# Optimization experiments

Hardware: AMD Instinct MI355X
Metric: run time of the kernel (lower is better)

Reference implementation:

```python
import jax, jax.numpy as jnp
import numpy as np

B, NUM, FEAT, H = 32, 512, 1024, 8
HLEN = FEAT // H  # 128


def setup_inputs() -> dict:
    key = jax.random.key(0)
    ks = jax.random.split(key, 9)
    x1 = jax.random.normal(ks[0], (B, NUM, FEAT), dtype=jnp.float32)
    x2 = jax.random.normal(ks[1], (B, NUM, FEAT), dtype=jnp.float32)
    adj = jax.random.uniform(ks[2], (B, NUM, NUM), dtype=jnp.float32)
    bias = jax.random.normal(ks[3], (B, NUM, NUM), dtype=jnp.float32)
    mask = jax.random.bernoulli(ks[4], 0.1, (B, 1, NUM, NUM))  # bool
    # per-head projection weights: FCNet([feat, hdim], '', 0.1) == Linear(feat, hdim)
    Wq = jax.random.normal(ks[5], (H, FEAT, HLEN), dtype=jnp.float32) * (1.0 / np.sqrt(FEAT))
    bq = jnp.zeros((H, HLEN), dtype=jnp.float32)
    # output FCNet([feat, feat], 'ReLU', 0.1) == Linear(feat, feat) + ReLU
    Wl = jax.random.normal(ks[6], (FEAT, FEAT), dtype=jnp.float32) * (1.0 / np.sqrt(FEAT))
    bl = jnp.zeros((FEAT,), dtype=jnp.float32)
    return {"x1": x1, "x2": x2, "adj": adj, "bias": bias, "mask": mask,
            "Wq": Wq, "bq": bq, "Wl": Wl, "bl": bl}


def reference(x1, x2, adj, bias, mask, Wq, bq, Wl, bl):
    # adj and bias are unused in the original forward.
    Bsz, num, feat = x1.shape
    h_len = feat // H
    # Q: concat of per-head Linear(feat, h_len) projections -> [B, num, feat],
    # then split into H heads of h_len: [B, H, num, h_len]
    Q = jnp.einsum('bnf,hfd->bhnd', x1, Wq) + bq[None, :, None, :]
    # K = V = x1 reshaped into heads
    K = x1.reshape(Bsz, num, H, h_len).transpose(0, 2, 1, 3)  # [B,H,num,h_len]
    V = K
    # gate: average pool x2 over its sequence dim -> [B, feat] -> [B,H,1,h_len]
    gate = jnp.mean(x2, axis=1).reshape(Bsz, 1, H, h_len).transpose(0, 2, 1, 3)
    scale = 1.0 / np.sqrt(float(h_len))
    aff = jnp.einsum('bhnd,bhmd->bhnm', Q * gate, K * gate) * scale
    L = jnp.where(mask, jnp.float32(-1e9), aff)
    att = jax.nn.softmax(L, axis=3)  # [B,H,num,num]
    V_ = jnp.einsum('bhnm,bhmd->bhnd', att, V)
    V_ = V_.transpose(0, 2, 1, 3).reshape(Bsz, num, feat)
    xout = jax.nn.relu(V_ @ Wl + bl) + x1
    return (xout, att)
```

## Files before the change

### kernel.cpp

```cpp
#include <hip/hip_runtime.h>
#include <hip/hip_bf16.h>

typedef __attribute__((ext_vector_type(8))) short s8v;
typedef __attribute__((ext_vector_type(4))) float f4v;
typedef __hip_bfloat16 bf16;

__device__ __forceinline__ unsigned short f2b(float f) {
  bf16 h = __float2bfloat16(f);
  return *reinterpret_cast<unsigned short*>(&h);
}

__device__ __forceinline__ void gload16(const void* g, void* l) {
  __builtin_amdgcn_global_load_lds(
      (const __attribute__((address_space(1))) void*)g,
      (__attribute__((address_space(3))) void*)l, 16, 0, 0);
}

__global__ __launch_bounds__(256) void gate_kernel(const float* __restrict__ x2,
                                                   float* __restrict__ g2s) {
  __shared__ float red[256];
  const int b = blockIdx.x >> 4, fc = blockIdx.x & 15;
  const int fi = threadIdx.x & 63, ng = threadIdx.x >> 6;
  const int f = fc * 64 + fi;
  const float* p = x2 + (size_t)b * 524288 + f;
  float s = 0.f;
  for (int n = ng * 128; n < ng * 128 + 128; ++n) s += p[(size_t)n * 1024];
  red[threadIdx.x] = s;
  __syncthreads();
  if (threadIdx.x < 64) {
    float tot = red[fi] + red[fi + 64] + red[fi + 128] + red[fi + 192];
    float mean = tot * (1.0f / 512.0f);
    g2s[b * 1024 + f] = mean * mean * 0.08838834764831845f;
  }
}

__global__ __launch_bounds__(256) void cvt_f32_bf16(const float* __restrict__ in,
                                                    bf16* __restrict__ out, int n4) {
  int i = blockIdx.x * 256 + threadIdx.x;
  if (i >= n4) return;
  f4v v = reinterpret_cast<const f4v*>(in)[i];
  ushort4 o;
  o.x = f2b(v.x); o.y = f2b(v.y); o.z = f2b(v.z); o.w = f2b(v.w);
  reinterpret_cast<ushort4*>(out)[i] = o;
}

__global__ __launch_bounds__(256) void transpose_f32_bf16(
    const float* __restrict__ in, bf16* __restrict__ out,
    int in_rstride, int out_rstride, int hi_shift,
    long hi_mul, long lo_mul, long out_mul) {
  __shared__ float tile[32][33];
  const int z = blockIdx.z;
  const long in_off = (long)(z >> hi_shift) * hi_mul + (long)(z & ((1 << hi_shift) - 1)) * lo_mul;
  const int r0 = blockIdx.x * 32, c0 = blockIdx.y * 32;
  const int i = threadIdx.x >> 5, j = threadIdx.x & 31;
  const float* ip = in + in_off + (long)r0 * in_rstride + c0;
#pragma unroll
  for (int s = 0; s < 4; ++s) tile[i + s * 8][j] = ip[(long)(i + s * 8) * in_rstride + j];
  __syncthreads();
  bf16* op = out + (long)z * out_mul + (long)c0 * out_rstride + r0;
#pragma unroll
  for (int s = 0; s < 4; ++s) op[(long)(i + s * 8) * out_rstride + j] = __float2bfloat16(tile[j][i + s * 8]);
}

template <int EPI>
__global__ __launch_bounds__(256) void gemm_nt(
    const bf16* __restrict__ A, const bf16* __restrict__ BT, void* __restrict__ Op,
    const float* __restrict__ e1, const float* __restrict__ e2) {
  __shared__ alignas(16) bf16 As[128 * 32];
  __shared__ alignas(16) bf16 Bs[128 * 32];
  const int t = threadIdx.x;
  const int lane = t & 63;
  const int wv = t >> 6;
  const int wr = wv >> 1, wc = wv & 1;
  const int lr = lane & 15, g = lane >> 4;
  const int o = blockIdx.x;
  const int wk = (o & 7) * 128 + (o >> 3);
  const int m0 = (wk >> 3) * 128, n0 = (wk & 7) * 128;

  const int cr = lane >> 2;
  const int q = (lane & 3) ^ ((lane >> 3) & 3);
  const int c0 = 2 * wv, c1 = 2 * wv + 1;
  const bf16* gA0 = A + (size_t)(m0 + c0 * 16 + cr) * 1024 + q * 8;
  const bf16* gA1 = A + (size_t)(m0 + c1 * 16 + cr) * 1024 + q * 8;
  const bf16* gB0 = BT + (size_t)(n0 + c0 * 16 + cr) * 1024 + q * 8;
  const bf16* gB1 = BT + (size_t)(n0 + c1 * 16 + cr) * 1024 + q * 8;
  bf16* lA0 = &As[c0 * 512]; bf16* lA1 = &As[c1 * 512];
  bf16* lB0 = &Bs[c0 * 512]; bf16* lB1 = &Bs[c1 * 512];

  f4v acc[4][4];
#pragma unroll
  for (int i = 0; i < 4; ++i)
#pragma unroll
    for (int j = 0; j < 4; ++j) acc[i][j] = (f4v){0.f, 0.f, 0.f, 0.f};

  const int xr = (lr >> 1) & 3;

  for (int k0 = 0; k0 < 1024; k0 += 32) {
    __syncthreads();
    gload16(gA0 + k0, lA0);
    gload16(gA1 + k0, lA1);
    gload16(gB0 + k0, lB0);
    gload16(gB1 + k0, lB1);
    __syncthreads();
    s8v af[4], bfr[4];
#pragma unroll
    for (int mi = 0; mi < 4; ++mi)
      af[mi] = *reinterpret_cast<const s8v*>(&As[(wr * 64 + mi * 16 + lr) * 32 + ((g ^ xr) * 8)]);
#pragma unroll
    for (int ni = 0; ni < 4; ++ni)
      bfr[ni] = *reinterpret_cast<const s8v*>(&Bs[(wc * 64 + ni * 16 + lr) * 32 + ((g ^ xr) * 8)]);
#pragma unroll
    for (int mi = 0; mi < 4; ++mi)
#pragma unroll
      for (int ni = 0; ni < 4; ++ni)
        acc[mi][ni] = __builtin_amdgcn_mfma_f32_16x16x32_bf16(af[mi], bfr[ni], acc[mi][ni], 0, 0, 0);
  }

#pragma unroll
  for (int mi = 0; mi < 4; ++mi) {
#pragma unroll
    for (int ni = 0; ni < 4; ++ni) {
#pragma unroll
      for (int v = 0; v < 4; ++v) {
        int row = m0 + wr * 64 + mi * 16 + g * 4 + v;
        int col = n0 + wc * 64 + ni * 16 + lr;
        float val = acc[mi][ni][v];
        if constexpr (EPI == 0) {
          float qv = (val + e1[col]) * e2[(row >> 9) * 1024 + col];
          reinterpret_cast<bf16*>(Op)[(size_t)row * 1024 + col] = __float2bfloat16(qv);
        } else {
          float r2 = fmaxf(val + e1[col], 0.f) + e2[(size_t)row * 1024 + col];
          reinterpret_cast<float*>(Op)[(size_t)row * 1024 + col] = r2;
        }
      }
    }
  }
}

__device__ __forceinline__ int fsw(int r) { return ((r >> 2) | ((r & 1) << 2)); }

__global__ __launch_bounds__(256) void attn_fused(
    const bf16* __restrict__ Qs, const bf16* __restrict__ x1b,
    const bf16* __restrict__ VT, const int* __restrict__ mask,
    float* __restrict__ att, bf16* __restrict__ Vout) {
  __shared__ bf16 P[4][16 * 512];
  const int o = blockIdx.x;
  const int wk = (o & 7) * 256 + (o >> 3);
  const int rt = wk & 7, bh = wk >> 3;
  const int h = bh & 7, b = bh >> 3;
  const int wv = threadIdx.x >> 6;
  const int lane = threadIdx.x & 63;
  const int lr = lane & 15, g = lane >> 4;
  const int n0 = rt * 64 + wv * 16;

  const bf16* qrow = Qs + (size_t)(b * 512 + n0 + lr) * 1024 + h * 128;
  s8v a[4];
#pragma unroll
  for (int kt = 0; kt < 4; ++kt) a[kt] = *reinterpret_cast<const s8v*>(qrow + kt * 32 + g * 8);

  f4v acc[32];
#pragma unroll
  for (int mt = 0; mt < 32; ++mt) acc[mt] = (f4v){0.f, 0.f, 0.f, 0.f};

  const bf16* kbase = x1b + (size_t)b * 524288 + h * 128;
#pragma unroll
  for (int mt = 0; mt < 32; ++mt) {
    const bf16* krow = kbase + (size_t)(mt * 16 + lr) * 1024;
#pragma unroll
    for (int kt = 0; kt < 4; ++kt) {
      s8v bb = *reinterpret_cast<const s8v*>(krow + kt * 32 + g * 8);
      acc[mt] = __builtin_amdgcn_mfma_f32_16x16x32_bf16(a[kt], bb, acc[mt], 0, 0, 0);
    }
  }

  const int* mrow = mask + (size_t)b * 262144 + (size_t)n0 * 512;
  float mx[4] = {-3e38f, -3e38f, -3e38f, -3e38f};
#pragma unroll
  for (int mt = 0; mt < 32; ++mt) {
#pragma unroll
    for (int v = 0; v < 4; ++v) {
      int row = g * 4 + v, col = mt * 16 + lr;
      float val = acc[mt][v];
      val = mrow[row * 512 + col] ? -1e9f : val;
      acc[mt][v] = val;
      mx[v] = fmaxf(mx[v], val);
    }
  }
#pragma unroll
  for (int v = 0; v < 4; ++v) {
    float m = mx[v];
    m = fmaxf(m, __shfl_xor(m, 1));
    m = fmaxf(m, __shfl_xor(m, 2));
    m = fmaxf(m, __shfl_xor(m, 4));
    m = fmaxf(m, __shfl_xor(m, 8));
    mx[v] = m;
  }
  float sm[4] = {0.f, 0.f, 0.f, 0.f};
#pragma unroll
  for (int mt = 0; mt < 32; ++mt) {
#pragma unroll
    for (int v = 0; v < 4; ++v) {
      float e = __expf(acc[mt][v] - mx[v]);
      acc[mt][v] = e;
      sm[v] += e;
    }
  }
#pragma unroll
  for (int v = 0; v < 4; ++v) {
    float s = sm[v];
    s += __shfl_xor(s, 1);
    s += __shfl_xor(s, 2);
    s += __shfl_xor(s, 4);
    s += __shfl_xor(s, 8);
    sm[v] = 1.0f / s;
  }

  float* orow = att + ((size_t)bh * 512 + n0) * 512;
  bf16* Pw = P[wv];
#pragma unroll
  for (int mt = 0; mt < 32; ++mt) {
#pragma unroll
    for (int v = 0; v < 4; ++v) {
      int r = g * 4 + v, c = mt * 16 + lr;
      float tv = acc[mt][v] * sm[v];
      orow[r * 512 + c] = tv;
      Pw[r * 512 + (c ^ (fsw(r) * 8))] = __float2bfloat16(tv);
    }
  }

  s8v a2[16];
  const int fx = fsw(lr) * 8;
#pragma unroll
  for (int kt = 0; kt < 16; ++kt)
    a2[kt] = *reinterpret_cast<const s8v*>(&Pw[lr * 512 + ((kt * 32 + g * 8) ^ fx)]);

  const bf16* vbase = VT + (size_t)bh * 65536;
#pragma unroll
  for (int nt = 0; nt < 8; ++nt) {
    f4v oacc = (f4v){0.f, 0.f, 0.f, 0.f};
#pragma unroll
    for (int kt = 0; kt < 16; ++kt) {
      s8v bb = *reinterpret_cast<const s8v*>(vbase + (size_t)(nt * 16 + lr) * 512 + kt * 32 + g * 8);
      oacc = __builtin_amdgcn_mfma_f32_16x16x32_bf16(a2[kt], bb, oacc, 0, 0, 0);
    }
#pragma unroll
    for (int v = 0; v < 4; ++v) {
      Vout[(size_t)(b * 512 + n0 + g * 4 + v) * 1024 + h * 128 + nt * 16 + lr] =
          __float2bfloat16(oacc[v]);
    }
  }
}

extern "C" void kernel_launch(void* const* d_in, const int* in_sizes, int n_in,
                              void* d_out, int out_size, void* d_ws, size_t ws_size,
                              hipStream_t stream) {
  (void)in_sizes; (void)n_in; (void)out_size; (void)ws_size;
  const float* x1 = (const float*)d_in[0];
  const float* x2 = (const float*)d_in[1];
  const int* mask = (const int*)d_in[4];
  const float* Wq = (const float*)d_in[5];
  const float* bq = (const float*)d_in[6];
  const float* Wl = (const float*)d_in[7];
  const float* bl = (const float*)d_in[8];

  float* xout = (float*)d_out;
  float* att = (float*)d_out + 16777216;

  char* ws = (char*)d_ws;
  bf16* x1b   = (bf16*)(ws);
  bf16* VT    = (bf16*)(ws + 33554432);
  bf16* Qs    = (bf16*)(ws + 67108864);
  bf16* WcatT = (bf16*)(ws + 100663296);
  bf16* WlT   = (bf16*)(ws + 102760448);
  float* g2s  = (float*)(ws + 104857600);

  gate_kernel<<<dim3(32 * 16), dim3(256), 0, stream>>>(x2, g2s);
  cvt_f32_bf16<<<dim3(16384), dim3(256), 0, stream>>>(x1, x1b, 4194304);
  transpose_f32_bf16<<<dim3(16, 4, 256), dim3(256), 0, stream>>>(
      x1, VT, 1024, 512, 3, (long)524288, (long)128, (long)65536);
  transpose_f32_bf16<<<dim3(32, 4, 8), dim3(256), 0, stream>>>(
      Wq, WcatT, 128, 1024, 0, (long)131072, (long)0, (long)131072);
  transpose_f32_bf16<<<dim3(32, 32, 1), dim3(256), 0, stream>>>(
      Wl, WlT, 1024, 1024, 0, (long)0, (long)0, (long)0);
  gemm_nt<0><<<dim3(1024), dim3(256), 0, stream>>>(x1b, WcatT, (void*)Qs, bq, g2s);
  attn_fused<<<dim3(2048), dim3(256), 0, stream>>>(Qs, x1b, VT, mask, att, Qs);
  gemm_nt<2><<<dim3(1024), dim3(256), 0, stream>>>(Qs, WlT, (void*)xout, bl, x1);
}
```

Baseline: 901.8 us.

## Stage K/V tiles through LDS, bit-pack mask, fuse x1 conversion passes

Fuses the x1 bf16 conversion and the V transpose into one kernel so x1 is read once. Adds a maskpack kernel that packs the int mask into per-lane bitwords, stored in the no-longer-needed WcatT workspace. The attention kernel now double-buffers K and V tiles into shared memory with swizzled global_load_lds, letting all four waves share those loads. For the PV product it reloads the just-written fp32 attention rows from global memory instead of keeping P in LDS. This adds a launch and extra syncs, and depends on the att stores being visible after __syncthreads.

New measurement: 809.6 us. 10.2% less time.

```diff
diff --git a/kernel.cpp b/kernel.cpp
--- a/kernel.cpp
+++ b/kernel.cpp
@@ -34,14 +34,27 @@
   }
 }
 
-__global__ __launch_bounds__(256) void cvt_f32_bf16(const float* __restrict__ in,
-                                                    bf16* __restrict__ out, int n4) {
-  int i = blockIdx.x * 256 + threadIdx.x;
-  if (i >= n4) return;
-  f4v v = reinterpret_cast<const f4v*>(in)[i];
-  ushort4 o;
-  o.x = f2b(v.x); o.y = f2b(v.y); o.z = f2b(v.z); o.w = f2b(v.w);
-  reinterpret_cast<ushort4*>(out)[i] = o;
+__global__ __launch_bounds__(256) void x1prep(const float* __restrict__ x1,
+                                              bf16* __restrict__ x1b,
+                                              bf16* __restrict__ VT) {
+  __shared__ float tile[32][33];
+  const int mt = blockIdx.x;
+  const int ft = blockIdx.y;
+  const int b = blockIdx.z;
+  const int i = threadIdx.x >> 5, j = threadIdx.x & 31;
+  const float* ip = x1 + (size_t)b * 524288 + (size_t)(mt * 32) * 1024 + ft * 32;
+#pragma unroll
+  for (int s = 0; s < 4; ++s) {
+    float v = ip[(size_t)(i + s * 8) * 1024 + j];
+    tile[i + s * 8][j] = v;
+    x1b[(size_t)(b * 512 + mt * 32 + i + s * 8) * 1024 + ft * 32 + j] = __float2bfloat16(v);
+  }
+  __syncthreads();
+  const int h = ft >> 2, d0 = (ft & 3) * 32;
+  bf16* op = VT + (size_t)(b * 8 + h) * 65536 + (size_t)d0 * 512 + mt * 32;
+#pragma unroll
+  for (int s = 0; s < 4; ++s)
+    op[(size_t)(i + s * 8) * 512 + j] = __float2bfloat16(tile[j][i + s * 8]);
 }
 
 __global__ __launch_bounds__(256) void transpose_f32_bf16(
@@ -60,6 +73,24 @@
   bf16* op = out + (long)z * out_mul + (long)c0 * out_rstride + r0;
 #pragma unroll
   for (int s = 0; s < 4; ++s) op[(long)(i + s * 8) * out_rstride + j] = __float2bfloat16(tile[j][i + s * 8]);
+}
+
+__global__ __launch_bounds__(256) void maskpack(const int* __restrict__ mask,
+                                                unsigned* __restrict__ mp) {
+  __shared__ int rb[4][512];
+  const int w = threadIdx.x >> 6, lane = threadIdx.x & 63;
+  const int row = blockIdx.x * 4 + w;
+  const int4* src = (const int4*)(mask + (size_t)row * 512);
+  int4 a = src[lane * 2], c = src[lane * 2 + 1];
+  *(int4*)&rb[w][lane * 8] = a;
+  *(int4*)&rb[w][lane * 8 + 4] = c;
+  __syncthreads();
+  if (lane < 16) {
+    unsigned wd = 0;
+#pragma unroll
+    for (int mt = 0; mt < 32; ++mt) wd |= (rb[w][mt * 16 + lane] ? 1u : 0u) << mt;
+    mp[(size_t)row * 16 + lane] = wd;
+  }
 }
 
 template <int EPI>
@@ -137,51 +168,85 @@
   }
 }
 
-__device__ __forceinline__ int fsw(int r) { return ((r >> 2) | ((r & 1) << 2)); }
-
 __global__ __launch_bounds__(256) void attn_fused(
     const bf16* __restrict__ Qs, const bf16* __restrict__ x1b,
-    const bf16* __restrict__ VT, const int* __restrict__ mask,
+    const bf16* __restrict__ VT, const unsigned* __restrict__ mp,
     float* __restrict__ att, bf16* __restrict__ Vout) {
-  __shared__ bf16 P[4][16 * 512];
+  __shared__ alignas(16) bf16 stage[2][8192];
   const int o = blockIdx.x;
   const int wk = (o & 7) * 256 + (o >> 3);
   const int rt = wk & 7, bh = wk >> 3;
   const int h = bh & 7, b = bh >> 3;
-  const int wv = threadIdx.x >> 6;
+  const int w = threadIdx.x >> 6;
   const int lane = threadIdx.x & 63;
   const int lr = lane & 15, g = lane >> 4;
-  const int n0 = rt * 64 + wv * 16;
+  const int n0 = rt * 64 + w * 16;
+
+  const bf16* kbase = x1b + (size_t)b * 524288 + h * 128;
+  const bf16* vbase = VT + (size_t)bh * 65536;
+  const int ks = lane & 15;
+  const int vs = lane & 7;
+  const int xf = lr & 7;
 
   const bf16* qrow = Qs + (size_t)(b * 512 + n0 + lr) * 1024 + h * 128;
-  s8v a[4];
-#pragma unroll
-  for (int kt = 0; kt < 4; ++kt) a[kt] = *reinterpret_cast<const s8v*>(qrow + kt * 32 + g * 8);
+  s8v qa[4];
+#pragma unroll
+  for (int kt = 0; kt < 4; ++kt) qa[kt] = *reinterpret_cast<const s8v*>(qrow + kt * 32 + g * 8);
+
+  unsigned mw[4];
+#pragma unroll
+  for (int v = 0; v < 4; ++v)
+    mw[v] = mp[(size_t)(b * 512 + n0 + g * 4 + v) * 16 + lr];
 
   f4v acc[32];
 #pragma unroll
   for (int mt = 0; mt < 32; ++mt) acc[mt] = (f4v){0.f, 0.f, 0.f, 0.f};
 
-  const bf16* kbase = x1b + (size_t)b * 524288 + h * 128;
+  auto STAGE_K = [&](int ck, int bufi) {
+#pragma unroll
+    for (int i = 0; i < 4; ++i) {
+      int r = (w * 4 + i) * 4 + (lane >> 4);
+      const bf16* src = kbase + (size_t)(ck * 64 + r) * 1024 + ((ks ^ (r & 7)) * 8);
+      gload16(src, &stage[bufi][(w * 4 + i) * 512]);
+    }
+  };
+  auto STAGE_V = [&](int cv, int bufi) {
+#pragma unroll
+    for (int i = 0; i < 4; ++i) {
+      int d = (w * 4 + i) * 8 + (lane >> 3);
+      const bf16* src = vbase + (size_t)d * 512 + cv * 64 + ((vs ^ (d & 7)) * 8);
+      gload16(src, &stage[bufi][(w * 4 + i) * 512]);
+    }
+  };
+
+  STAGE_K(0, 0);
+  __syncthreads();
+#pragma unroll
+  for (int t = 0; t < 8; ++t) {
+    if (t < 7) STAGE_K(t + 1, (t + 1) & 1);
+    else       STAGE_V(0, 0);
+    const bf16* bufp = stage[t & 1];
+#pragma unroll
+    for (int mtl = 0; mtl < 4; ++mtl) {
+#pragma unroll
+      for (int kt = 0; kt < 4; ++kt) {
+        s8v bb = *reinterpret_cast<const s8v*>(
+            bufp + (mtl * 16 + lr) * 128 + (((kt * 4 + g) ^ xf) * 8));
+        acc[t * 4 + mtl] =
+            __builtin_amdgcn_mfma_f32_16x16x32_bf16(qa[kt], bb, acc[t * 4 + mtl], 0, 0, 0);
+      }
+    }
+    __syncthreads();
+  }
+  STAGE_V(1, 1);
+
+  float mx[4] = {-3e38f, -3e38f, -3e38f, -3e38f};
 #pragma unroll
   for (int mt = 0; mt < 32; ++mt) {
-    const bf16* krow = kbase + (size_t)(mt * 16 + lr) * 1024;
-#pragma unroll
-    for (int kt = 0; kt < 4; ++kt) {
-      s8v bb = *reinterpret_cast<const s8v*>(krow + kt * 32 + g * 8);
-      acc[mt] = __builtin_amdgcn_mfma_f32_16x16x32_bf16(a[kt], bb, acc[mt], 0, 0, 0);
-    }
-  }
-
-  const int* mrow = mask + (size_t)b * 262144 + (size_t)n0 * 512;
-  float mx[4] = {-3e38f, -3e38f, -3e38f, -3e38f};
-#pragma unroll
-  for (int mt = 0; mt < 32; ++mt) {
 #pragma unroll
     for (int v = 0; v < 4; ++v) {
-      int row = g * 4 + v, col = mt * 16 + lr;
       float val = acc[mt][v];
-      val = mrow[row * 512 + col] ? -1e9f : val;
+      val = ((mw[v] >> mt) & 1u) ? -1e9f : val;
       acc[mt][v] = val;
       mx[v] = fmaxf(mx[v], val);
     }
@@ -216,37 +281,54 @@
   }
 
   float* orow = att + ((size_t)bh * 512 + n0) * 512;
-  bf16* Pw = P[wv];
 #pragma unroll
   for (int mt = 0; mt < 32; ++mt) {
 #pragma unroll
-    for (int v = 0; v < 4; ++v) {
-      int r = g * 4 + v, c = mt * 16 + lr;
-      float tv = acc[mt][v] * sm[v];
-      orow[r * 512 + c] = tv;
-      Pw[r * 512 + (c ^ (fsw(r) * 8))] = __float2bfloat16(tv);
-    }
-  }
-
-  s8v a2[16];
-  const int fx = fsw(lr) * 8;
-#pragma unroll
-  for (int kt = 0; kt < 16; ++kt)
-    a2[kt] = *reinterpret_cast<const s8v*>(&Pw[lr * 512 + ((kt * 32 + g * 8) ^ fx)]);
-
-  const bf16* vbase = VT + (size_t)bh * 65536;
+    for (int v = 0; v < 4; ++v)
+      orow[(g * 4 + v) * 512 + mt * 16 + lr] = acc[mt][v] * sm[v];
+  }
+  __syncthreads();
+
+  f4v oacc[8];
+#pragma unroll
+  for (int nt = 0; nt < 8; ++nt) oacc[nt] = (f4v){0.f, 0.f, 0.f, 0.f};
+  const float* attq = att + ((size_t)bh * 512 + n0 + lr) * 512;
+
+#pragma unroll
+  for (int c = 0; c < 8; ++c) {
+    if (c >= 1 && c < 7) STAGE_V(c + 1, (c + 1) & 1);
+    const bf16* bufp = stage[c & 1];
+    s8v pa[2];
+#pragma unroll
+    for (int j = 0; j < 2; ++j) {
+      int kt = c * 2 + j;
+      f4v lo = *reinterpret_cast<const f4v*>(attq + kt * 32 + g * 8);
+      f4v hi = *reinterpret_cast<const f4v*>(attq + kt * 32 + g * 8 + 4);
+      s8v p;
+      p[0] = (short)f2b(lo.x); p[1] = (short)f2b(lo.y);
+      p[2] = (short)f2b(lo.z); p[3] = (short)f2b(lo.w);
+      p[4] = (short)f2b(hi.x); p[5] = (short)f2b(hi.y);
+      p[6] = (short)f2b(hi.z); p[7] = (short)f2b(hi.w);
+      pa[j] = p;
+    }
+#pragma unroll
+    for (int nt = 0; nt < 8; ++nt) {
+#pragma unroll
+      for (int j = 0; j < 2; ++j) {
+        s8v bb = *reinterpret_cast<const s8v*>(
+            bufp + (nt * 16 + lr) * 64 + (((j * 4 + g) ^ xf) * 8));
+        oacc[nt] = __builtin_amdgcn_mfma_f32_16x16x32_bf16(pa[j], bb, oacc[nt], 0, 0, 0);
+      }
+    }
+    __syncthreads();
+  }
+
 #pragma unroll
   for (int nt = 0; nt < 8; ++nt) {
-    f4v oacc = (f4v){0.f, 0.f, 0.f, 0.f};
-#pragma unroll
-    for (int kt = 0; kt < 16; ++kt) {
-      s8v bb = *reinterpret_cast<const s8v*>(vbase + (size_t)(nt * 16 + lr) * 512 + kt * 32 + g * 8);
-      oacc = __builtin_amdgcn_mfma_f32_16x16x32_bf16(a2[kt], bb, oacc, 0, 0, 0);
-    }
 #pragma unroll
     for (int v = 0; v < 4; ++v) {
       Vout[(size_t)(b * 512 + n0 + g * 4 + v) * 1024 + h * 128 + nt * 16 + lr] =
-          __float2bfloat16(oacc[v]);
+          __float2bfloat16(oacc[nt][v]);
     }
   }
 }
@@ -273,16 +355,16 @@
   bf16* WcatT = (bf16*)(ws + 100663296);
   bf16* WlT   = (bf16*)(ws + 102760448);
   float* g2s  = (float*)(ws + 104857600);
+  unsigned* mp = (unsigned*)WcatT;
 
   gate_kernel<<<dim3(32 * 16), dim3(256), 0, stream>>>(x2, g2s);
-  cvt_f32_bf16<<<dim3(16384), dim3(256), 0, stream>>>(x1, x1b, 4194304);
-  transpose_f32_bf16<<<dim3(16, 4, 256), dim3(256), 0, stream>>>(
-      x1, VT, 1024, 512, 3, (long)524288, (long)128, (long)65536);
+  x1prep<<<dim3(16, 32, 32), dim3(256), 0, stream>>>(x1, x1b, VT);
   transpose_f32_bf16<<<dim3(32, 4, 8), dim3(256), 0, stream>>>(
       Wq, WcatT, 128, 1024, 0, (long)131072, (long)0, (long)131072);
   transpose_f32_bf16<<<dim3(32, 32, 1), dim3(256), 0, stream>>>(
       Wl, WlT, 1024, 1024, 0, (long)0, (long)0, (long)0);
   gemm_nt<0><<<dim3(1024), dim3(256), 0, stream>>>(x1b, WcatT, (void*)Qs, bq, g2s);
-  attn_fused<<<dim3(2048), dim3(256), 0, stream>>>(Qs, x1b, VT, mask, att, Qs);
+  maskpack<<<dim3(4096), dim3(256), 0, stream>>>(mask, mp);
+  attn_fused<<<dim3(2048), dim3(256), 0, stream>>>(Qs, x1b, VT, mp, att, Qs);
   gemm_nt<2><<<dim3(1024), dim3(256), 0, stream>>>(Qs, WlT, (void*)xout, bl, x1);
 }
```
